# Kernel tuning notes

Measured on AMD Instinct MI355X. Metric: run time of the kernel, lower is better.

Reference implementation:

```python
import jax, jax.numpy as jnp
import numpy as np

B, IN, H, L = 4096, 1024, 1024, 8


def setup_inputs() -> dict:
    key = jax.random.key(0)
    k1, k2, k3, k4, k5 = jax.random.split(key, 5)
    scale = 0.02
    inputs = jax.random.normal(k1, (B, IN), dtype=jnp.float32)
    # Stacked gate weights, order [f, i, o, g] along first axis (torch Linear: y = x @ W.T + b)
    W = jax.random.normal(k2, (4 * H, IN), dtype=jnp.float32) * scale   # input->gates
    bW = jax.random.normal(k3, (4 * H,), dtype=jnp.float32) * scale
    U = jax.random.normal(k4, (4 * H, H), dtype=jnp.float32) * scale    # hidden->gates
    bU = jax.random.normal(k5, (4 * H,), dtype=jnp.float32) * scale
    return {"inputs": inputs, "W": W, "bW": bW, "U": U, "bU": bU, "num_layers": L}


def reference(inputs, W, bW, U, bU, num_layers):
    batch = inputs.shape[0]
    hid = U.shape[1]
    # Input projection is loop-invariant: compute once. [B, 4H]
    x_proj = jnp.einsum('bi,gi->bg', inputs, W) + bW
    xf, xi, xo, xg = jnp.split(x_proj, 4, axis=1)

    def step(carry, _):
        ht, ct = carry
        h_proj = jnp.einsum('bh,gh->bg', ht, U) + bU  # [B, 4H]
        hf, hi, ho, hg = jnp.split(h_proj, 4, axis=1)
        f = jax.nn.sigmoid(xf + hf)
        i = jax.nn.sigmoid(xi + hi)
        o = jax.nn.sigmoid(xo + ho)
        g = jnp.tanh(xg + hg)
        ct_new = f * ct + i * g
        ht_new = o * jnp.tanh(ct_new)
        return (ht_new, ct_new), None

    h0 = jnp.zeros((batch, hid), dtype=inputs.dtype)
    c0 = jnp.zeros((batch, hid), dtype=inputs.dtype)
    (ht, ct), _ = jax.lax.scan(step, (h0, c0), None, length=num_layers)
    return ht, ct
```

## Files before the change

kernel.cpp:

```cpp
#include <hip/hip_runtime.h>
#include <hip/hip_bf16.h>

typedef __bf16 bf16x8 __attribute__((ext_vector_type(8)));
typedef float f32x4 __attribute__((ext_vector_type(4)));
typedef long i64x2 __attribute__((ext_vector_type(2)));

#define DEVI static __device__ __forceinline__

DEVI void load_lds16(const void* g, void* l) {
  __builtin_amdgcn_global_load_lds(
      (const __attribute__((address_space(1))) void*)g,
      (__attribute__((address_space(3))) void*)l, 16, 0, 0);
}

DEVI unsigned short f2b(float f) { return __bfloat16_as_ushort(__float2bfloat16(f)); }
DEVI float b2f(unsigned short u) {
  union { unsigned int i; float f; } c;
  c.i = ((unsigned int)u) << 16;
  return c.f;
}
DEVI float sigm(float x) { return 1.0f / (1.0f + __expf(-x)); }
DEVI float tanh_fast(float x) { return 2.0f / (1.0f + __expf(-2.0f * x)) - 1.0f; }

DEVI unsigned char f2fp8(float f) {
  const unsigned int u = __float_as_uint(f);
  const unsigned char s = (unsigned char)((u >> 24) & 0x80);
  const float a = fabsf(f);
  if (a >= 448.f) return s | 0x7E;
  if (a < 0.015625f) {
    const int M = (int)rintf(a * 512.f);
    if (M > 7) return s | 0x08;
    return s | (unsigned char)M;
  }
  int ex;
  const float m = frexpf(a, &ex);
  int r = (int)rintf(m * 16.f);
  if (r == 16) { r = 8; ex += 1; }
  const int E = ex + 6, M = r - 8;
  if (E > 15 || (E == 15 && M == 7)) return s | 0x7E;
  return s | (unsigned char)((E << 3) | M);
}

DEVI int swz(int L) { return L ^ (((L >> 7) & 7) << 4); }

DEVI int imgk(int hc) {
  return (hc & ~63) + (((hc >> 3) & 3) << 4) + (((hc >> 5) & 1) << 3) + (hc & 7);
}

__global__ __launch_bounds__(256) void prep_kernel(
    const float* __restrict__ x, const float* __restrict__ W,
    const float* __restrict__ U, const float* __restrict__ bW,
    const float* __restrict__ bU, unsigned short* __restrict__ xb,
    unsigned short* __restrict__ Wbp, unsigned char* __restrict__ Up8,
    float* __restrict__ bp) {
  const int bid = blockIdx.x;
  if (bid < 4096) {
    const int i = bid * 256 + threadIdx.x;
    const float4 v = reinterpret_cast<const float4*>(x)[i];
    ushort4 o;
    o.x = f2b(v.x); o.y = f2b(v.y); o.z = f2b(v.z); o.w = f2b(v.w);
    reinterpret_cast<ushort4*>(xb)[i] = o;
  } else if (bid < 8192) {
    const int i = (bid - 4096) * 256 + threadIdx.x;
    const int r = i >> 8;
    const int cw = i & 255;
    const float4 v = reinterpret_cast<const float4*>(W)[i];
    const int rp = ((r & 1023) << 2) + (r >> 10);
    ushort4 o;
    o.x = f2b(v.x); o.y = f2b(v.y); o.z = f2b(v.z); o.w = f2b(v.w);
    *reinterpret_cast<ushort4*>(&Wbp[(size_t)rp * 1024 + (cw << 2)]) = o;
  } else if (bid < 9216) {
    const int i = (bid - 8192) * 256 + threadIdx.x;
    const int d0 = i << 4;
    const int rp = d0 >> 10;
    const int ik0 = d0 & 1023;
    const int P = ik0 >> 6, q = (ik0 >> 4) & 3;
    const int k0 = P * 64 + q * 8;
    const int srcrow = (rp & 3) * 1024 + (rp >> 2);
    const float* S = U + (size_t)srcrow * 1024;
    const float4 a0 = *reinterpret_cast<const float4*>(S + k0);
    const float4 a1 = *reinterpret_cast<const float4*>(S + k0 + 4);
    const float4 b0 = *reinterpret_cast<const float4*>(S + k0 + 32);
    const float4 b1 = *reinterpret_cast<const float4*>(S + k0 + 36);
    auto pk = [](unsigned char a, unsigned char b, unsigned char c, unsigned char d) {
      return (unsigned)a | ((unsigned)b << 8) | ((unsigned)c << 16) | ((unsigned)d << 24);
    };
    uint4 w;
    w.x = pk(f2fp8(a0.x * 32.f), f2fp8(a0.y * 32.f), f2fp8(a0.z * 32.f), f2fp8(a0.w * 32.f));
    w.y = pk(f2fp8(a1.x * 32.f), f2fp8(a1.y * 32.f), f2fp8(a1.z * 32.f), f2fp8(a1.w * 32.f));
    w.z = pk(f2fp8(b0.x * 32.f), f2fp8(b0.y * 32.f), f2fp8(b0.z * 32.f), f2fp8(b0.w * 32.f));
    w.w = pk(f2fp8(b1.x * 32.f), f2fp8(b1.y * 32.f), f2fp8(b1.z * 32.f), f2fp8(b1.w * 32.f));
    *reinterpret_cast<uint4*>(&Up8[d0]) = w;
  } else {
    const int i = (bid - 9216) * 256 + threadIdx.x;
    const int h = i >> 2, g = i & 3;
    bp[i] = bW[g * 1024 + h] + bU[g * 1024 + h];
  }
}

#define KPHASE(BFC, BFN, SLNXT, STAGEQ, DOSTAGE, WAITSTR, DOBAR)              \
  {                                                                           \
    if (DOSTAGE) STAGE(STAGEQ);                                               \
    const unsigned char* sln_ = (SLNXT);                                      \
    _Pragma("unroll") for (int n_ = 0; n_ < 4; ++n_)                          \
        BFN[n_] = *reinterpret_cast<const bf16x8*>(sln_ + offB[n_]);          \
    __builtin_amdgcn_s_setprio(1);                                            \
    _Pragma("unroll") for (int m_ = 0; m_ < 8; ++m_) {                        \
      _Pragma("unroll") for (int n_ = 0; n_ < 4; ++n_)                        \
          acc[m_][n_] = __builtin_amdgcn_mfma_f32_16x16x32_bf16(              \
              af[m_], BFC[n_], acc[m_][n_], 0, 0, 0);                         \
      af[m_] = *reinterpret_cast<const bf16x8*>(sln_ + offA[m_]);             \
    }                                                                         \
    __builtin_amdgcn_s_setprio(0);                                            \
    asm volatile(WAITSTR ::: "memory");                                       \
    __builtin_amdgcn_sched_barrier(0);                                        \
    if (DOBAR) {                                                              \
      __builtin_amdgcn_s_barrier();                                           \
      __builtin_amdgcn_sched_barrier(0);                                      \
    }                                                                         \
  }

__global__ __launch_bounds__(512, 2) void gemm_x(
    const unsigned short* __restrict__ A,
    const unsigned short* __restrict__ Bm,
    unsigned short* __restrict__ xpb_w,
    const float* __restrict__ bp,
    unsigned short* __restrict__ ct,
    unsigned char* __restrict__ htimg) {
  constexpr int K = 1024, N = 4096;
  __shared__ unsigned char lds[256 * 528];

  const int tid = threadIdx.x;
  const int lane = tid & 63;
  const int wave = tid >> 6;
  const int wr = wave >> 2, wc = wave & 3;
  const int bid = blockIdx.x;
  const int sw = (bid & 7) * 32 + (bid >> 3);
  const int brow = (sw >> 4) * 256, bcol = (sw & 15) * 256;

  const int physA0 = tid * 16, physA1 = 8192 + tid * 16;
  const int physB0 = 16384 + tid * 16, physB1 = 24576 + tid * 16;
  const int LA0 = swz(physA0);
  const int LA1r = swz(8192 + tid * 16);
  const int LB0 = swz(tid * 16), LB1 = swz(8192 + tid * 16);
  const unsigned char* pA0 = (const unsigned char*)A + (size_t)(brow + (LA0 >> 6)) * (K * 2) + (LA0 & 63);
  const unsigned char* pA1 = (const unsigned char*)A + (size_t)(brow + (LA1r >> 6)) * (K * 2) + (LA1r & 63);
  const unsigned char* pB0 = (const unsigned char*)Bm + (size_t)(bcol + (LB0 >> 6)) * (K * 2) + (LB0 & 63);
  const unsigned char* pB1 = (const unsigned char*)Bm + (size_t)(bcol + (LB1 >> 6)) * (K * 2) + (LB1 & 63);

  const int s16 = (lane >> 4) * 16;
  int offA[8], offB[4];
#pragma unroll
  for (int m = 0; m < 8; ++m)
    offA[m] = swz((wr * 128 + m * 16 + (lane & 15)) * 64 + s16);
#pragma unroll
  for (int n = 0; n < 4; ++n)
    offB[n] = 16384 + swz((wc * 64 + n * 16 + (lane & 15)) * 64 + s16);

  f32x4 acc[8][4] = {};
  bf16x8 af[8], bfE[4], bfO[4];

  auto STAGE = [&](int q) {
    unsigned char* sb = lds + (q & 3) * 32768;
    const size_t kb = (size_t)q * 64;
    load_lds16(pA0 + kb, sb + physA0);
    load_lds16(pA1 + kb, sb + physA1);
    load_lds16(pB0 + kb, sb + physB0);
    load_lds16(pB1 + kb, sb + physB1);
  };

  STAGE(0); STAGE(1); STAGE(2); STAGE(3);
  asm volatile("s_waitcnt vmcnt(8)" ::: "memory");
  __builtin_amdgcn_s_barrier();
#pragma unroll
  for (int n = 0; n < 4; ++n) bfE[n] = *reinterpret_cast<const bf16x8*>(lds + offB[n]);
#pragma unroll
  for (int m = 0; m < 8; ++m) af[m] = *reinterpret_cast<const bf16x8*>(lds + offA[m]);
  asm volatile("s_waitcnt lgkmcnt(0)" ::: "memory");
  __builtin_amdgcn_sched_barrier(0);
  __builtin_amdgcn_s_barrier();
  __builtin_amdgcn_sched_barrier(0);

  for (int pp = 0; pp < 14; ++pp) {
    const int p = 2 * pp;
    const unsigned char* sl1 = lds + ((p + 1) & 3) * 32768;
    const unsigned char* sl2 = lds + ((p + 2) & 3) * 32768;
    KPHASE(bfE, bfO, sl1, p + 4, true, "s_waitcnt vmcnt(8) lgkmcnt(0)", true);
    KPHASE(bfO, bfE, sl2, p + 5, true, "s_waitcnt vmcnt(8) lgkmcnt(0)", true);
  }
  KPHASE(bfE, bfO, lds + (29 & 3) * 32768, 0, false, "s_waitcnt vmcnt(4) lgkmcnt(0)", true);
  KPHASE(bfO, bfE, lds + (30 & 3) * 32768, 0, false, "s_waitcnt vmcnt(0) lgkmcnt(0)", true);
  KPHASE(bfE, bfO, lds + (31 & 3) * 32768, 0, false, "s_waitcnt lgkmcnt(0)", false);
  __builtin_amdgcn_s_setprio(1);
#pragma unroll
  for (int m = 0; m < 8; ++m)
#pragma unroll
    for (int n = 0; n < 4; ++n)
      acc[m][n] = __builtin_amdgcn_mfma_f32_16x16x32_bf16(af[m], bfO[n], acc[m][n], 0, 0, 0);
  __builtin_amdgcn_s_setprio(0);

  __syncthreads();
  unsigned short* cs = (unsigned short*)lds;
  {
    const int c0 = wc * 64 + (lane & 15);
    const int r00 = wr * 128 + ((lane >> 4) << 2);
#pragma unroll
    for (int m = 0; m < 8; ++m)
#pragma unroll
      for (int n = 0; n < 4; ++n) {
        const int rr = r00 + m * 16, cc = c0 + n * 16;
#pragma unroll
        for (int r = 0; r < 4; ++r) cs[(rr + r) * 264 + cc] = f2b(acc[m][n][r]);
      }
  }
  __syncthreads();

  const int hbase = bcol >> 2;
#pragma unroll 2
  for (int j = 0; j < 8; ++j) {
    const int v = tid + (j << 9);
    const int row = v >> 4;
    const int h4 = (v & 15) << 2;
    const int ci = (brow + row) * 1024 + hbase + h4;

    unsigned short pvv[16];
    *reinterpret_cast<uint4*>(&pvv[0]) = *reinterpret_cast<const uint4*>(&cs[row * 264 + h4 * 4]);
    *reinterpret_cast<uint4*>(&pvv[8]) = *reinterpret_cast<const uint4*>(&cs[row * 264 + h4 * 4 + 8]);

    float bpf[16];
#pragma unroll
    for (int q = 0; q < 4; ++q)
      *reinterpret_cast<float4*>(&bpf[q * 4]) =
          *reinterpret_cast<const float4*>(&bp[bcol + h4 * 4 + q * 4]);

    float sf[4], si_[4], so_[4], sg_[4];
    unsigned short xo[16];
#pragma unroll
    for (int k = 0; k < 4; ++k) {
      sf[k] = b2f(pvv[4 * k + 0]) + bpf[4 * k + 0];
      si_[k] = b2f(pvv[4 * k + 1]) + bpf[4 * k + 1];
      so_[k] = b2f(pvv[4 * k + 2]) + bpf[4 * k + 2];
      sg_[k] = b2f(pvv[4 * k + 3]) + bpf[4 * k + 3];
      xo[4 * k + 0] = f2b(sf[k]);
      xo[4 * k + 1] = f2b(si_[k]);
      xo[4 * k + 2] = f2b(so_[k]);
      xo[4 * k + 3] = f2b(sg_[k]);
    }
    unsigned short* xw = &xpb_w[(size_t)(brow + row) * N + bcol + h4 * 4];
    *reinterpret_cast<uint4*>(xw) = *reinterpret_cast<const uint4*>(&xo[0]);
    *reinterpret_cast<uint4*>(xw + 8) = *reinterpret_cast<const uint4*>(&xo[8]);

    float cn[4], hn[4];
#pragma unroll
    for (int k = 0; k < 4; ++k) {
      const float ii = sigm(si_[k]);
      const float o = sigm(so_[k]);
      const float gg = tanh_fast(sg_[k]);
      const float c = ii * gg;
      cn[k] = c;
      hn[k] = o * tanh_fast(c);
    }
    ushort4 cb;
    cb.x = f2b(cn[0]); cb.y = f2b(cn[1]); cb.z = f2b(cn[2]); cb.w = f2b(cn[3]);
    *reinterpret_cast<ushort4*>(&ct[ci]) = cb;
    const int hc0 = hbase + h4;
    uchar4 h8;
    h8.x = f2fp8(hn[0] * 16.f); h8.y = f2fp8(hn[1] * 16.f);
    h8.z = f2fp8(hn[2] * 16.f); h8.w = f2fp8(hn[3] * 16.f);
    *reinterpret_cast<uchar4*>(&htimg[(size_t)(brow + row) * 1024 + imgk(hc0)]) = h8;
  }
}

#define KPHASE8(BFC, BFN, SLNXT, STAGEQ, DOSTAGE, WAITSTR, DOBAR)             \
  {                                                                           \
    if (DOSTAGE) STAGE(STAGEQ);                                               \
    const unsigned char* sln_ = (SLNXT);                                      \
    _Pragma("unroll") for (int n_ = 0; n_ < 4; ++n_)                          \
        BFN[n_] = *reinterpret_cast<const i64x2*>(sln_ + offB[n_]);           \
    __builtin_amdgcn_s_setprio(1);                                            \
    _Pragma("unroll") for (int m_ = 0; m_ < 4; ++m_) {                        \
      _Pragma("unroll") for (int n_ = 0; n_ < 4; ++n_)                        \
          acc[m_][n_] = __builtin_amdgcn_mfma_f32_16x16x32_fp8_fp8(           \
              af[m_][0], BFC[n_][0], acc[m_][n_], 0, 0, 0);                   \
      _Pragma("unroll") for (int n_ = 0; n_ < 4; ++n_)                        \
          acc[m_][n_] = __builtin_amdgcn_mfma_f32_16x16x32_fp8_fp8(           \
              af[m_][1], BFC[n_][1], acc[m_][n_], 0, 0, 0);                   \
      af[m_] = *reinterpret_cast<const i64x2*>(sln_ + offA[m_]);              \
    }                                                                         \
    __builtin_amdgcn_s_setprio(0);                                            \
    asm volatile(WAITSTR ::: "memory");                                       \
    __builtin_amdgcn_sched_barrier(0);                                        \
    if (DOBAR) {                                                              \
      __builtin_amdgcn_s_barrier();                                           \
      __builtin_amdgcn_sched_barrier(0);                                      \
    }                                                                         \
  }

template <bool LAST>
__global__ __launch_bounds__(256, 3) void gemm_r(
    const unsigned char* __restrict__ Aimg,
    const unsigned char* __restrict__ Bimg,
    const unsigned short* __restrict__ xpb_r,
    unsigned short* __restrict__ ct,
    unsigned char* __restrict__ htimg,
    float* __restrict__ out) {
  constexpr int N = 4096;
  constexpr int SLOT = 16384;
  __shared__ unsigned char lds[3 * SLOT];

  const int tid = threadIdx.x;
  const int lane = tid & 63;
  const int wave = tid >> 6;
  const int wr = wave >> 1, wc = wave & 1;
  const int bid = blockIdx.x;
  const int sw = (bid & 7) * 128 + (bid >> 3);
  const int brow = (sw >> 5) * 128, bcol = (sw & 31) * 128;

  const int physA0 = tid * 16, physA1 = 4096 + tid * 16;
  const int physB0 = 8192 + tid * 16, physB1 = 12288 + tid * 16;
  const int LA0 = swz(tid * 16), LA1 = swz(4096 + tid * 16);
  const unsigned char* pA0 = Aimg + (size_t)(brow + (LA0 >> 6)) * 1024 + (LA0 & 63);
  const unsigned char* pA1 = Aimg + (size_t)(brow + (LA1 >> 6)) * 1024 + (LA1 & 63);
  const unsigned char* pB0 = Bimg + (size_t)(bcol + (LA0 >> 6)) * 1024 + (LA0 & 63);
  const unsigned char* pB1 = Bimg + (size_t)(bcol + (LA1 >> 6)) * 1024 + (LA1 & 63);

  const int s16 = (lane >> 4) * 16;
  int offA[4], offB[4];
#pragma unroll
  for (int m = 0; m < 4; ++m)
    offA[m] = swz((wr * 64 + m * 16 + (lane & 15)) * 64 + s16);
#pragma unroll
  for (int n = 0; n < 4; ++n)
    offB[n] = 8192 + swz((wc * 64 + n * 16 + (lane & 15)) * 64 + s16);

  f32x4 acc[4][4] = {};
  i64x2 af[4], bfE[4], bfO[4];

  auto STAGE = [&](int q) {
    unsigned char* sb = lds + (q % 3) * SLOT;
    const size_t kb = (size_t)q * 64;
    load_lds16(pA0 + kb, sb + physA0);
    load_lds16(pA1 + kb, sb + physA1);
    load_lds16(pB0 + kb, sb + physB0);
    load_lds16(pB1 + kb, sb + physB1);
  };

  STAGE(0); STAGE(1); STAGE(2);
  asm volatile("s_waitcnt vmcnt(4)" ::: "memory");
  __builtin_amdgcn_s_barrier();
#pragma unroll
  for (int n = 0; n < 4; ++n) bfE[n] = *reinterpret_cast<const i64x2*>(lds + offB[n]);
#pragma unroll
  for (int m = 0; m < 4; ++m) af[m] = *reinterpret_cast<const i64x2*>(lds + offA[m]);
  asm volatile("s_waitcnt lgkmcnt(0)" ::: "memory");
  __builtin_amdgcn_sched_barrier(0);
  __builtin_amdgcn_s_barrier();
  __builtin_amdgcn_sched_barrier(0);

  for (int pp = 0; pp < 6; ++pp) {
    const int p = 2 * pp;
    const unsigned char* sl1 = lds + ((p + 1) % 3) * SLOT;
    const unsigned char* sl2 = lds + ((p + 2) % 3) * SLOT;
    KPHASE8(bfE, bfO, sl1, p + 3, true, "s_waitcnt vmcnt(4) lgkmcnt(0)", true);
    KPHASE8(bfO, bfE, sl2, p + 4, true, "s_waitcnt vmcnt(4) lgkmcnt(0)", true);
  }
  KPHASE8(bfE, bfO, lds + (13 % 3) * SLOT, 15, true, "s_waitcnt vmcnt(4) lgkmcnt(0)", true);
  KPHASE8(bfO, bfE, lds + (14 % 3) * SLOT, 0, false, "s_waitcnt vmcnt(0) lgkmcnt(0)", true);
  KPHASE8(bfE, bfO, lds + (15 % 3) * SLOT, 0, false, "s_waitcnt lgkmcnt(0)", false);
  __builtin_amdgcn_s_setprio(1);
#pragma unroll
  for (int m = 0; m < 4; ++m) {
#pragma unroll
    for (int n = 0; n < 4; ++n)
      acc[m][n] = __builtin_amdgcn_mfma_f32_16x16x32_fp8_fp8(af[m][0], bfO[n][0], acc[m][n], 0, 0, 0);
#pragma unroll
    for (int n = 0; n < 4; ++n)
      acc[m][n] = __builtin_amdgcn_mfma_f32_16x16x32_fp8_fp8(af[m][1], bfO[n][1], acc[m][n], 0, 0, 0);
  }
  __builtin_amdgcn_s_setprio(0);

  __syncthreads();
  unsigned short* cs = (unsigned short*)lds;
  {
    const float inv = 1.0f / 512.0f;
    const int c0 = wc * 64 + (lane & 15);
    const int r00 = wr * 64 + ((lane >> 4) << 2);
#pragma unroll
    for (int m = 0; m < 4; ++m)
#pragma unroll
      for (int n = 0; n < 4; ++n) {
        const int rr = r00 + m * 16, cc = c0 + n * 16;
#pragma unroll
        for (int r = 0; r < 4; ++r) cs[(rr + r) * 132 + cc] = f2b(acc[m][n][r] * inv);
      }
  }
  __syncthreads();

  const int hbase = bcol >> 2;
#pragma unroll 2
  for (int j = 0; j < 4; ++j) {
    const int v = tid + (j << 8);
    const int row = v >> 3;
    const int h4 = (v & 7) << 2;
    const int ci = (brow + row) * 1024 + hbase + h4;

    unsigned short pvv[16], xvv[16];
    *reinterpret_cast<uint4*>(&pvv[0]) = *reinterpret_cast<const uint4*>(&cs[row * 132 + h4 * 4]);
    *reinterpret_cast<uint4*>(&pvv[8]) = *reinterpret_cast<const uint4*>(&cs[row * 132 + h4 * 4 + 8]);
    const unsigned short* xr = &xpb_r[(size_t)(brow + row) * N + bcol + h4 * 4];
    *reinterpret_cast<uint4*>(&xvv[0]) = *reinterpret_cast<const uint4*>(xr);
    *reinterpret_cast<uint4*>(&xvv[8]) = *reinterpret_cast<const uint4*>(xr + 8);

    const ushort4 cv = *reinterpret_cast<const ushort4*>(&ct[ci]);
    float c_old[4] = {b2f(cv.x), b2f(cv.y), b2f(cv.z), b2f(cv.w)};

    float cn[4], hn[4];
#pragma unroll
    for (int k = 0; k < 4; ++k) {
      const float f = sigm(b2f(pvv[4 * k + 0]) + b2f(xvv[4 * k + 0]));
      const float ii = sigm(b2f(pvv[4 * k + 1]) + b2f(xvv[4 * k + 1]));
      const float o = sigm(b2f(pvv[4 * k + 2]) + b2f(xvv[4 * k + 2]));
      const float gg = tanh_fast(b2f(pvv[4 * k + 3]) + b2f(xvv[4 * k + 3]));
      const float c = fmaf(f, c_old[k], ii * gg);
      cn[k] = c;
      hn[k] = o * tanh_fast(c);
    }

    if constexpr (LAST) {
      *reinterpret_cast<float4*>(&out[ci]) = make_float4(hn[0], hn[1], hn[2], hn[3]);
      *reinterpret_cast<float4*>(&out[4194304 + ci]) = make_float4(cn[0], cn[1], cn[2], cn[3]);
    } else {
      ushort4 cb;
      cb.x = f2b(cn[0]); cb.y = f2b(cn[1]); cb.z = f2b(cn[2]); cb.w = f2b(cn[3]);
      *reinterpret_cast<ushort4*>(&ct[ci]) = cb;
      const int hc0 = hbase + h4;
      uchar4 h8;
      h8.x = f2fp8(hn[0] * 16.f); h8.y = f2fp8(hn[1] * 16.f);
      h8.z = f2fp8(hn[2] * 16.f); h8.w = f2fp8(hn[3] * 16.f);
      *reinterpret_cast<uchar4*>(&htimg[(size_t)(brow + row) * 1024 + imgk(hc0)]) = h8;
    }
  }
}

extern "C" void kernel_launch(void* const* d_in, const int* in_sizes, int n_in,
                              void* d_out, int out_size, void* d_ws, size_t ws_size,
                              hipStream_t stream) {
  const float* x = (const float*)d_in[0];
  const float* W = (const float*)d_in[1];
  const float* bW = (const float*)d_in[2];
  const float* U = (const float*)d_in[3];
  const float* bU = (const float*)d_in[4];
  float* out = (float*)d_out;

  char* w = (char*)d_ws;
  const size_t MB = 1ull << 20;
  unsigned short* xb = (unsigned short*)(w + 0 * MB);
  unsigned short* Wbp = (unsigned short*)(w + 8 * MB);
  unsigned char* Up8 = (unsigned char*)(w + 16 * MB);
  unsigned short* xpb = (unsigned short*)(w + 24 * MB);
  unsigned short* ct = (unsigned short*)(w + 56 * MB);
  unsigned char* htA = (unsigned char*)(w + 64 * MB);
  unsigned char* htB = (unsigned char*)(w + 68 * MB);
  float* bp = (float*)(w + 72 * MB);

  prep_kernel<<<9232, 256, 0, stream>>>(x, W, U, bW, bU, xb, Wbp, Up8, bp);

  gemm_x<<<256, 512, 0, stream>>>(xb, Wbp, xpb, bp, ct, htA);

  const unsigned char* hin = htA;
  unsigned char* hout = htB;
  for (int t = 1; t <= 6; ++t) {
    gemm_r<false><<<1024, 256, 0, stream>>>(hin, Up8, xpb, ct, hout, nullptr);
    const unsigned char* tmp = hout;
    hout = (unsigned char*)hin;
    hin = tmp;
  }
  gemm_r<true><<<1024, 256, 0, stream>>>(hin, Up8, xpb, ct, nullptr, out);
}
```

Measured before the change: 350.2 us.

## Shrink gemm_x tiles to 128x128 with 4 waves and triple-buffered LDS

The input-projection GEMM kernel moves from 256x256 tiles with 8 waves and a 4-slot LDS ring to 128x128 tiles with 4 waves and a 3-slot ring. The grid grows from 256 to 1024 blocks, and launch bounds allow 3 blocks per CU. This targets a grid of only 256 blocks, which underfills a CU-rich GPU, and it raises occupancy to hide latency. In exchange each block reuses less data, so global traffic per flop goes up, and the K pipeline is rescheduled with modulo-3 slot indexing.

```diff
diff --git a/kernel.cpp b/kernel.cpp
--- a/kernel.cpp
+++ b/kernel.cpp
@@ -98,14 +98,14 @@
   }
 }
 
-#define KPHASE(BFC, BFN, SLNXT, STAGEQ, DOSTAGE, WAITSTR, DOBAR)              \
+#define KPHASEX(BFC, BFN, SLNXT, STAGEQ, DOSTAGE, WAITSTR, DOBAR)             \
   {                                                                           \
     if (DOSTAGE) STAGE(STAGEQ);                                               \
     const unsigned char* sln_ = (SLNXT);                                      \
     _Pragma("unroll") for (int n_ = 0; n_ < 4; ++n_)                          \
         BFN[n_] = *reinterpret_cast<const bf16x8*>(sln_ + offB[n_]);          \
     __builtin_amdgcn_s_setprio(1);                                            \
-    _Pragma("unroll") for (int m_ = 0; m_ < 8; ++m_) {                        \
+    _Pragma("unroll") for (int m_ = 0; m_ < 4; ++m_) {                        \
       _Pragma("unroll") for (int n_ = 0; n_ < 4; ++n_)                        \
           acc[m_][n_] = __builtin_amdgcn_mfma_f32_16x16x32_bf16(              \
               af[m_], BFC[n_], acc[m_][n_], 0, 0, 0);                         \
@@ -120,48 +120,48 @@
     }                                                                         \
   }
 
-__global__ __launch_bounds__(512, 2) void gemm_x(
+__global__ __launch_bounds__(256, 3) void gemm_x(
     const unsigned short* __restrict__ A,
     const unsigned short* __restrict__ Bm,
     unsigned short* __restrict__ xpb_w,
     const float* __restrict__ bp,
     unsigned short* __restrict__ ct,
     unsigned char* __restrict__ htimg) {
-  constexpr int K = 1024, N = 4096;
-  __shared__ unsigned char lds[256 * 528];
+  constexpr int N = 4096;
+  constexpr int NPH = 32;
+  constexpr int SLOT = 16384;
+  __shared__ unsigned char lds[3 * SLOT];
 
   const int tid = threadIdx.x;
   const int lane = tid & 63;
   const int wave = tid >> 6;
-  const int wr = wave >> 2, wc = wave & 3;
+  const int wr = wave >> 1, wc = wave & 1;
   const int bid = blockIdx.x;
-  const int sw = (bid & 7) * 32 + (bid >> 3);
-  const int brow = (sw >> 4) * 256, bcol = (sw & 15) * 256;
-
-  const int physA0 = tid * 16, physA1 = 8192 + tid * 16;
-  const int physB0 = 16384 + tid * 16, physB1 = 24576 + tid * 16;
-  const int LA0 = swz(physA0);
-  const int LA1r = swz(8192 + tid * 16);
-  const int LB0 = swz(tid * 16), LB1 = swz(8192 + tid * 16);
-  const unsigned char* pA0 = (const unsigned char*)A + (size_t)(brow + (LA0 >> 6)) * (K * 2) + (LA0 & 63);
-  const unsigned char* pA1 = (const unsigned char*)A + (size_t)(brow + (LA1r >> 6)) * (K * 2) + (LA1r & 63);
-  const unsigned char* pB0 = (const unsigned char*)Bm + (size_t)(bcol + (LB0 >> 6)) * (K * 2) + (LB0 & 63);
-  const unsigned char* pB1 = (const unsigned char*)Bm + (size_t)(bcol + (LB1 >> 6)) * (K * 2) + (LB1 & 63);
+  const int sw = (bid & 7) * 128 + (bid >> 3);
+  const int brow = (sw >> 5) * 128, bcol = (sw & 31) * 128;
+
+  const int physA0 = tid * 16, physA1 = 4096 + tid * 16;
+  const int physB0 = 8192 + tid * 16, physB1 = 12288 + tid * 16;
+  const int LA0 = swz(tid * 16), LA1 = swz(4096 + tid * 16);
+  const unsigned char* pA0 = (const unsigned char*)A + (size_t)(brow + (LA0 >> 6)) * 2048 + (LA0 & 63);
+  const unsigned char* pA1 = (const unsigned char*)A + (size_t)(brow + (LA1 >> 6)) * 2048 + (LA1 & 63);
+  const unsigned char* pB0 = (const unsigned char*)Bm + (size_t)(bcol + (LA0 >> 6)) * 2048 + (LA0 & 63);
+  const unsigned char* pB1 = (const unsigned char*)Bm + (size_t)(bcol + (LA1 >> 6)) * 2048 + (LA1 & 63);
 
   const int s16 = (lane >> 4) * 16;
-  int offA[8], offB[4];
-#pragma unroll
-  for (int m = 0; m < 8; ++m)
-    offA[m] = swz((wr * 128 + m * 16 + (lane & 15)) * 64 + s16);
+  int offA[4], offB[4];
+#pragma unroll
+  for (int m = 0; m < 4; ++m)
+    offA[m] = swz((wr * 64 + m * 16 + (lane & 15)) * 64 + s16);
 #pragma unroll
   for (int n = 0; n < 4; ++n)
-    offB[n] = 16384 + swz((wc * 64 + n * 16 + (lane & 15)) * 64 + s16);
-
-  f32x4 acc[8][4] = {};
-  bf16x8 af[8], bfE[4], bfO[4];
+    offB[n] = 8192 + swz((wc * 64 + n * 16 + (lane & 15)) * 64 + s16);
+
+  f32x4 acc[4][4] = {};
+  bf16x8 af[4], bfE[4], bfO[4];
 
   auto STAGE = [&](int q) {
-    unsigned char* sb = lds + (q & 3) * 32768;
+    unsigned char* sb = lds + (q % 3) * SLOT;
     const size_t kb = (size_t)q * 64;
     load_lds16(pA0 + kb, sb + physA0);
     load_lds16(pA1 + kb, sb + physA1);
@@ -169,13 +169,13 @@
     load_lds16(pB1 + kb, sb + physB1);
   };
 
-  STAGE(0); STAGE(1); STAGE(2); STAGE(3);
-  asm volatile("s_waitcnt vmcnt(8)" ::: "memory");
+  STAGE(0); STAGE(1); STAGE(2);
+  asm volatile("s_waitcnt vmcnt(4)" ::: "memory");
   __builtin_amdgcn_s_barrier();
 #pragma unroll
   for (int n = 0; n < 4; ++n) bfE[n] = *reinterpret_cast<const bf16x8*>(lds + offB[n]);
 #pragma unroll
-  for (int m = 0; m < 8; ++m) af[m] = *reinterpret_cast<const bf16x8*>(lds + offA[m]);
+  for (int m = 0; m < 4; ++m) af[m] = *reinterpret_cast<const bf16x8*>(lds + offA[m]);
   asm volatile("s_waitcnt lgkmcnt(0)" ::: "memory");
   __builtin_amdgcn_sched_barrier(0);
   __builtin_amdgcn_s_barrier();
@@ -183,17 +183,17 @@
 
   for (int pp = 0; pp < 14; ++pp) {
     const int p = 2 * pp;
-    const unsigned char* sl1 = lds + ((p + 1) & 3) * 32768;
-    const unsigned char* sl2 = lds + ((p + 2) & 3) * 32768;
-    KPHASE(bfE, bfO, sl1, p + 4, true, "s_waitcnt vmcnt(8) lgkmcnt(0)", true);
-    KPHASE(bfO, bfE, sl2, p + 5, true, "s_waitcnt vmcnt(8) lgkmcnt(0)", true);
-  }
-  KPHASE(bfE, bfO, lds + (29 & 3) * 32768, 0, false, "s_waitcnt vmcnt(4) lgkmcnt(0)", true);
-  KPHASE(bfO, bfE, lds + (30 & 3) * 32768, 0, false, "s_waitcnt vmcnt(0) lgkmcnt(0)", true);
-  KPHASE(bfE, bfO, lds + (31 & 3) * 32768, 0, false, "s_waitcnt lgkmcnt(0)", false);
+    const unsigned char* sl1 = lds + ((p + 1) % 3) * SLOT;
+    const unsigned char* sl2 = lds + ((p + 2) % 3) * SLOT;
+    KPHASEX(bfE, bfO, sl1, p + 3, true, "s_waitcnt vmcnt(4) lgkmcnt(0)", true);
+    KPHASEX(bfO, bfE, sl2, p + 4, true, "s_waitcnt vmcnt(4) lgkmcnt(0)", true);
+  }
+  KPHASEX(bfE, bfO, lds + (29 % 3) * SLOT, 31, true, "s_waitcnt vmcnt(4) lgkmcnt(0)", true);
+  KPHASEX(bfO, bfE, lds + (30 % 3) * SLOT, 0, false, "s_waitcnt vmcnt(0) lgkmcnt(0)", true);
+  KPHASEX(bfE, bfO, lds + (31 % 3) * SLOT, 0, false, "s_waitcnt lgkmcnt(0)", false);
   __builtin_amdgcn_s_setprio(1);
 #pragma unroll
-  for (int m = 0; m < 8; ++m)
+  for (int m = 0; m < 4; ++m)
 #pragma unroll
     for (int n = 0; n < 4; ++n)
       acc[m][n] = __builtin_amdgcn_mfma_f32_16x16x32_bf16(af[m], bfO[n], acc[m][n], 0, 0, 0);
@@ -203,29 +203,29 @@
   unsigned short* cs = (unsigned short*)lds;
   {
     const int c0 = wc * 64 + (lane & 15);
-    const int r00 = wr * 128 + ((lane >> 4) << 2);
-#pragma unroll
-    for (int m = 0; m < 8; ++m)
+    const int r00 = wr * 64 + ((lane >> 4) << 2);
+#pragma unroll
+    for (int m = 0; m < 4; ++m)
 #pragma unroll
       for (int n = 0; n < 4; ++n) {
         const int rr = r00 + m * 16, cc = c0 + n * 16;
 #pragma unroll
-        for (int r = 0; r < 4; ++r) cs[(rr + r) * 264 + cc] = f2b(acc[m][n][r]);
+        for (int r = 0; r < 4; ++r) cs[(rr + r) * 132 + cc] = f2b(acc[m][n][r]);
       }
   }
   __syncthreads();
 
   const int hbase = bcol >> 2;
 #pragma unroll 2
-  for (int j = 0; j < 8; ++j) {
-    const int v = tid + (j << 9);
-    const int row = v >> 4;
-    const int h4 = (v & 15) << 2;
+  for (int j = 0; j < 4; ++j) {
+    const int v = tid + (j << 8);
+    const int row = v >> 3;
+    const int h4 = (v & 7) << 2;
     const int ci = (brow + row) * 1024 + hbase + h4;
 
     unsigned short pvv[16];
-    *reinterpret_cast<uint4*>(&pvv[0]) = *reinterpret_cast<const uint4*>(&cs[row * 264 + h4 * 4]);
-    *reinterpret_cast<uint4*>(&pvv[8]) = *reinterpret_cast<const uint4*>(&cs[row * 264 + h4 * 4 + 8]);
+    *reinterpret_cast<uint4*>(&pvv[0]) = *reinterpret_cast<const uint4*>(&cs[row * 132 + h4 * 4]);
+    *reinterpret_cast<uint4*>(&pvv[8]) = *reinterpret_cast<const uint4*>(&cs[row * 132 + h4 * 4 + 8]);
 
     float bpf[16];
 #pragma unroll
@@ -465,7 +465,7 @@
 
   prep_kernel<<<9232, 256, 0, stream>>>(x, W, U, bW, bU, xb, Wbp, Up8, bp);
 
-  gemm_x<<<256, 512, 0, stream>>>(xb, Wbp, xpb, bp, ct, htA);
+  gemm_x<<<1024, 256, 0, stream>>>(xb, Wbp, xpb, bp, ct, htA);
 
   const unsigned char* hin = htA;
   unsigned char* hout = htB;
```

Result: no change. 351.4 us (+0.3%).
